# Performance work log

Hardware: AMD Instinct MI355X
Metric: run time of the kernel (lower is better)

## Reference

```python
import jax, jax.numpy as jnp
import numpy as np

TILE = 128  # pixel tile size, matches tile_pixels=128 default


def setup_inputs() -> dict:
    key = jax.random.key(0)
    ks = jax.random.split(key, 24)
    C, H, W, A, D, N, NC = 512, 32, 32, 256, 512, 1024, 30
    p = lambda k, s: (jax.random.normal(k, s, dtype=jnp.float32) * 0.02)
    return {
        "enc_out_nchw": jax.random.normal(ks[0], (1, C, H, W), dtype=jnp.float32),
        "tag_H": jax.random.normal(ks[1], (N, D), dtype=jnp.float32),
        # CellAttention linears ([in,out] layout)
        "W_enc": p(ks[2], (C, A)), "b_enc": p(ks[3], (A,)),
        "W_tag": p(ks[4], (D, A)), "b_tag": p(ks[5], (A,)),
        "W_lang": p(ks[6], (D, A)), "b_lang": p(ks[7], (A,)),
        "w_full": p(ks[8], (A,)), "b_full": p(ks[9], ()),
        # init hidden / gate
        "W_init": p(ks[10], (C, D)), "b_init": p(ks[11], (D,)),
        "W_fbeta": p(ks[12], (D, C)), "b_fbeta": p(ks[13], (C,)),
        # heads
        "W_cls": p(ks[14], (C, NC + 1)), "b_cls": p(ks[15], (NC + 1,)),
        "W_m1": p(ks[16], (C, 256)), "b_m1": p(ks[17], (256,)),
        "W_m2": p(ks[18], (256, 256)), "b_m2": p(ks[19], (256,)),
        "W_m3": p(ks[20], (256, 4)), "b_m3": p(ks[21], (4,)),
    }


def reference(enc_out_nchw, tag_H, W_enc, b_enc, W_tag, b_tag, W_lang, b_lang,
              w_full, b_full, W_init, b_init, W_fbeta, b_fbeta,
              W_cls, b_cls, W_m1, b_m1, W_m2, b_m2, W_m3, b_m3):
    C = enc_out_nchw.shape[1]
    enc_flat = enc_out_nchw[0].reshape(C, -1).T          # [P, C]
    P = enc_flat.shape[0]
    N = tag_H.shape[0]

    S_p = enc_flat @ W_enc + b_enc                       # [P, A]
    R_n = tag_H @ W_tag + b_tag                          # [N, A]
    mean_enc = enc_flat.mean(axis=0)                     # [C]
    h0 = mean_enc @ W_init + b_init                      # [D] (same row expanded to N in torch)
    L = h0 @ W_lang + b_lang                             # [A] (identical for all cells)
    RL = R_n + L                                         # [N, A]

    # tiled additive-attention scores; never materialize [N,P,A]
    T = P // TILE
    Sp_tiles = S_p.reshape(T, TILE, -1)                  # [T, TILE, A]

    def tile_score(_, sp_tile):
        z = jax.nn.relu(RL[:, None, :] + sp_tile[None, :, :]) @ w_full + b_full  # [N, TILE]
        return None, z

    _, Z = jax.lax.scan(tile_score, None, Sp_tiles)      # [T, N, TILE]
    Z = jnp.transpose(Z, (1, 0, 2)).reshape(N, P)        # [N, P]

    alpha = jax.nn.softmax(Z, axis=1)                    # streaming softmax == stable softmax
    awe = alpha @ enc_flat                               # [N, C]

    gate = jax.nn.sigmoid(h0 @ W_fbeta + b_fbeta)        # [C]
    h = gate * awe * h0                                  # [N, C]; dropout is identity at inference

    logits_cls = h @ W_cls + b_cls                       # [N, num_classes+1]
    x = jax.nn.relu(h @ W_m1 + b_m1)
    x = jax.nn.relu(x @ W_m2 + b_m2)
    boxes = jax.nn.sigmoid(x @ W_m3 + b_m3)              # [N, 4]
    return logits_cls, boxes
```

## Files before the change

kernel.cpp:

```cpp
#include <hip/hip_runtime.h>
#include <math.h>


__device__ __forceinline__ float4 ld4(const float* p) {
  return *reinterpret_cast<const float4*>(p);
}
__device__ __forceinline__ void st4(float* p, float4 v) {
  *reinterpret_cast<float4*>(p) = v;
}

__global__ void mean_kernel(const float* __restrict__ enc, float* __restrict__ mean) {
  const int c = blockIdx.x, t = threadIdx.x;
  float4 v = reinterpret_cast<const float4*>(enc + (size_t)c * 1024)[t];
  float s = v.x + v.y + v.z + v.w;
  #pragma unroll
  for (int off = 32; off; off >>= 1) s += __shfl_xor(s, off);
  __shared__ float red[4];
  if ((t & 63) == 0) red[t >> 6] = s;
  __syncthreads();
  if (t == 0) mean[c] = (red[0] + red[1] + red[2] + red[3]) * (1.0f / 1024.0f);
}

__global__ __launch_bounds__(256) void h0_k(
    const float* __restrict__ mean, const float* __restrict__ W_init,
    const float* __restrict__ b_init, float* __restrict__ h0) {
  __shared__ float ms[512];
  __shared__ float red[8][33];
  const int t = threadIdx.x;
  ms[t] = mean[t]; ms[t + 256] = mean[t + 256];
  __syncthreads();
  const int d0 = blockIdx.x * 32, dl = t & 31, cg = t >> 5;
  float acc = 0.f;
  #pragma unroll 8
  for (int c = cg * 64; c < cg * 64 + 64; ++c)
    acc += ms[c] * W_init[c * 512 + d0 + dl];
  red[cg][dl] = acc;
  __syncthreads();
  if (t < 32) {
    const float s = red[0][t] + red[1][t] + red[2][t] + red[3][t]
                  + red[4][t] + red[5][t] + red[6][t] + red[7][t];
    h0[d0 + t] = s + b_init[d0 + t];
  }
}

__global__ __launch_bounds__(256) void ghL_k(
    const float* __restrict__ h0, const float* __restrict__ W_fbeta,
    const float* __restrict__ b_fbeta, const float* __restrict__ W_lang,
    const float* __restrict__ b_lang, float* __restrict__ gh,
    float* __restrict__ Lv) {
  __shared__ float hs[512];
  __shared__ float red[8][33];
  const int t = threadIdx.x;
  hs[t] = h0[t]; hs[t + 256] = h0[t + 256];
  __syncthreads();
  const int b = blockIdx.x, ol = t & 31, cg = t >> 5;
  if (b < 16) {
    const int c0 = b * 32;
    float acc = 0.f;
    #pragma unroll 8
    for (int d = cg * 64; d < cg * 64 + 64; ++d)
      acc += hs[d] * W_fbeta[d * 512 + c0 + ol];
    red[cg][ol] = acc;
    __syncthreads();
    if (t < 32) {
      const int c = c0 + t;
      const float s = red[0][t] + red[1][t] + red[2][t] + red[3][t]
                    + red[4][t] + red[5][t] + red[6][t] + red[7][t] + b_fbeta[c];
      gh[c] = hs[c] / (1.f + __expf(-s));
    }
  } else {
    const int a0 = (b - 16) * 32;
    float acc = 0.f;
    #pragma unroll 8
    for (int d = cg * 64; d < cg * 64 + 64; ++d)
      acc += hs[d] * W_lang[d * 256 + a0 + ol];
    red[cg][ol] = acc;
    __syncthreads();
    if (t < 32) {
      const float s = red[0][t] + red[1][t] + red[2][t] + red[3][t]
                    + red[4][t] + red[5][t] + red[6][t] + red[7][t];
      Lv[a0 + t] = s + b_lang[a0 + t];
    }
  }
}

template <int AMODE, int BMODE, bool BIAS1, bool NEXACT>
__device__ __forceinline__ void gemm_body2(
    const float* __restrict__ A0, const float* __restrict__ A1,
    const float* __restrict__ A2, const float* __restrict__ A3,
    const float* __restrict__ avec, const float* __restrict__ B,
    const float* __restrict__ bias1, float* __restrict__ C,
    int M, int N, int K, int m0, int n0, int k0, int nsteps,
    float* As, float* Bs) {
  constexpr int LDA = 36, LDB = 68, NA = 8, NB = 16;
  const int tid = threadIdx.x;
  const int tx = tid & 15, ty = tid >> 4;
  float acc[2][4] = {{0.f, 0.f, 0.f, 0.f}, {0.f, 0.f, 0.f, 0.f}};
  float pa[NA], pb[NB];

  auto loadA = [&](int kk0) {
    #pragma unroll
    for (int i = 0; i < NA; ++i) {
      const int idx = tid + i * 256;
      if (AMODE == 1) {
        const int k = idx >> 5, mm = idx & 31;
        pa[i] = A0[(size_t)(kk0 + k) * M + m0 + mm];
      } else {
        const int k = idx & 63, mm = idx >> 6;
        const size_t off = (size_t)(m0 + mm) * K + kk0 + k;
        if (AMODE == 0) {
          pa[i] = A0[off];
        } else {
          float s = A0[off] + A1[off] + A2[off] + A3[off];
          if (AMODE == 2) pa[i] = avec[kk0 + k] * s;
          else            pa[i] = fmaxf(s + avec[kk0 + k], 0.f);
        }
      }
    }
  };
  auto loadB = [&](int kk0) {
    #pragma unroll
    for (int i = 0; i < NB; ++i) {
      const int idx = tid + i * 256;
      if (BMODE == 0) {
        const int k = idx >> 6, nn = idx & 63;
        pb[i] = (NEXACT || (n0 + nn < N)) ? B[(size_t)(kk0 + k) * N + n0 + nn] : 0.f;
      } else {
        const int k = idx & 63, nn = idx >> 6;
        pb[i] = B[(size_t)(n0 + nn) * K + kk0 + k];
      }
    }
  };
  auto storeAB = [&]() {
    #pragma unroll
    for (int i = 0; i < NA; ++i) {
      const int idx = tid + i * 256;
      if (AMODE == 1) { const int k = idx >> 5, mm = idx & 31; As[k * LDA + mm] = pa[i]; }
      else            { const int k = idx & 63, mm = idx >> 6; As[k * LDA + mm] = pa[i]; }
    }
    #pragma unroll
    for (int i = 0; i < NB; ++i) {
      const int idx = tid + i * 256;
      if (BMODE == 0) { const int k = idx >> 6, nn = idx & 63; Bs[k * LDB + nn] = pb[i]; }
      else            { const int k = idx & 63, nn = idx >> 6; Bs[k * LDB + nn] = pb[i]; }
    }
  };

  loadA(k0); loadB(k0);
  for (int ts = 0; ts < nsteps; ++ts) {
    storeAB();
    __syncthreads();
    if (ts + 1 < nsteps) { loadA(k0 + (ts + 1) * 64); loadB(k0 + (ts + 1) * 64); }
    #pragma unroll
    for (int k = 0; k < 64; ++k) {
      const float2 av = *reinterpret_cast<const float2*>(As + k * LDA + ty * 2);
      const float4 bv = *reinterpret_cast<const float4*>(Bs + k * LDB + tx * 4);
      acc[0][0] += av.x * bv.x; acc[0][1] += av.x * bv.y;
      acc[0][2] += av.x * bv.z; acc[0][3] += av.x * bv.w;
      acc[1][0] += av.y * bv.x; acc[1][1] += av.y * bv.y;
      acc[1][2] += av.y * bv.z; acc[1][3] += av.y * bv.w;
    }
    __syncthreads();
  }

  #pragma unroll
  for (int i = 0; i < 2; ++i) {
    const int mm = m0 + ty * 2 + i;
    #pragma unroll
    for (int j = 0; j < 4; ++j) {
      const int nn = n0 + tx * 4 + j;
      if (NEXACT || nn < N) {
        float v = acc[i][j];
        if (BIAS1) v += bias1[nn];
        C[(size_t)mm * N + nn] = v;
      }
    }
  }
}

template <int AMODE, int BMODE>
__device__ __forceinline__ void gemm_body4(
    const float* __restrict__ A0, const float* __restrict__ A1,
    const float* __restrict__ A2, const float* __restrict__ A3,
    const float* __restrict__ avec, const float* __restrict__ B,
    float* __restrict__ C,
    int M, int N, int K, int m0, int n0, int k0, int nsteps,
    float* As, float* Bs) {
  constexpr int LD = 68, NA = 16, NB = 16;
  const int tid = threadIdx.x;
  const int tx = tid & 15, ty = tid >> 4;
  float acc[4][4];
  #pragma unroll
  for (int i = 0; i < 4; ++i)
    #pragma unroll
    for (int j = 0; j < 4; ++j) acc[i][j] = 0.f;
  float pa[NA], pb[NB];

  auto loadA = [&](int kk0) {
    #pragma unroll
    for (int i = 0; i < NA; ++i) {
      const int idx = tid + i * 256;
      if (AMODE == 1) {
        const int k = idx >> 6, mm = idx & 63;
        pa[i] = A0[(size_t)(kk0 + k) * M + m0 + mm];
      } else {
        const int k = idx & 63, mm = idx >> 6;
        const size_t off = (size_t)(m0 + mm) * K + kk0 + k;
        if (AMODE == 0) {
          pa[i] = A0[off];
        } else {
          float s = A0[off] + A1[off] + A2[off] + A3[off];
          if (AMODE == 2) pa[i] = avec[kk0 + k] * s;
          else            pa[i] = fmaxf(s + avec[kk0 + k], 0.f);
        }
      }
    }
  };
  auto loadB = [&](int kk0) {
    #pragma unroll
    for (int i = 0; i < NB; ++i) {
      const int idx = tid + i * 256;
      if (BMODE == 0) {
        const int k = idx >> 6, nn = idx & 63;
        pb[i] = B[(size_t)(kk0 + k) * N + n0 + nn];
      } else {
        const int k = idx & 63, nn = idx >> 6;
        pb[i] = B[(size_t)(n0 + nn) * K + kk0 + k];
      }
    }
  };
  auto storeAB = [&]() {
    #pragma unroll
    for (int i = 0; i < NA; ++i) {
      const int idx = tid + i * 256;
      if (AMODE == 1) { const int k = idx >> 6, mm = idx & 63; As[k * LD + mm] = pa[i]; }
      else            { const int k = idx & 63, mm = idx >> 6; As[k * LD + mm] = pa[i]; }
    }
    #pragma unroll
    for (int i = 0; i < NB; ++i) {
      const int idx = tid + i * 256;
      if (BMODE == 0) { const int k = idx >> 6, nn = idx & 63; Bs[k * LD + nn] = pb[i]; }
      else            { const int k = idx & 63, nn = idx >> 6; Bs[k * LD + nn] = pb[i]; }
    }
  };

  loadA(k0); loadB(k0);
  for (int ts = 0; ts < nsteps; ++ts) {
    storeAB();
    __syncthreads();
    if (ts + 1 < nsteps) { loadA(k0 + (ts + 1) * 64); loadB(k0 + (ts + 1) * 64); }
    #pragma unroll
    for (int k = 0; k < 64; ++k) {
      const float4 av = *reinterpret_cast<const float4*>(As + k * LD + ty * 4);
      const float4 bv = *reinterpret_cast<const float4*>(Bs + k * LD + tx * 4);
      const float a4[4] = {av.x, av.y, av.z, av.w};
      const float b4[4] = {bv.x, bv.y, bv.z, bv.w};
      #pragma unroll
      for (int i = 0; i < 4; ++i)
        #pragma unroll
        for (int j = 0; j < 4; ++j) acc[i][j] += a4[i] * b4[j];
    }
    __syncthreads();
  }

  #pragma unroll
  for (int i = 0; i < 4; ++i) {
    const int mm = m0 + ty * 4 + i;
    float4 v; v.x = acc[i][0]; v.y = acc[i][1]; v.z = acc[i][2]; v.w = acc[i][3];
    st4(C + (size_t)mm * N + n0 + tx * 4, v);
  }
}

#define GEMM_LDS __shared__ float As[64 * 68]; __shared__ float Bs[64 * 68]

__global__ __launch_bounds__(256) void sprl2(
    const float* __restrict__ enc, const float* __restrict__ W_enc,
    const float* __restrict__ tagH, const float* __restrict__ W_tag,
    float* __restrict__ PS, float* __restrict__ PR) {
  GEMM_LDS;
  const int b = blockIdx.x;
  if (b < 256) {
    const int tile = b & 63, c = b >> 6;
    const int mi = tile & 3, ni = tile >> 2;
    gemm_body4<1, 0>(W_enc, nullptr, nullptr, nullptr, nullptr, enc,
        PS + c * 262144, 256, 1024, 512, mi * 64, ni * 64, c * 128, 2, As, Bs);
  } else {
    const int r = b - 256, tile = r & 63, c = r >> 6;
    const int mi = tile >> 2, ni = tile & 3;
    gemm_body4<0, 0>(tagH, nullptr, nullptr, nullptr, nullptr, W_tag,
        PR + c * 262144, 1024, 256, 512, mi * 64, ni * 64, c * 128, 2, As, Bs);
  }
}

__global__ void merge_k(const float* __restrict__ PS, const float* __restrict__ PR,
                        const float* __restrict__ b_enc, const float* __restrict__ b_tag,
                        const float* __restrict__ Lv, float* __restrict__ Sp,
                        float* __restrict__ RLm) {
  const int b = blockIdx.x, t = threadIdx.x;
  if (b < 256) {
    const size_t a = ((size_t)b * 256 + t) * 4;
    float4 s0 = ld4(PS + a), s1 = ld4(PS + 262144 + a);
    float4 s2 = ld4(PS + 524288 + a), s3 = ld4(PS + 786432 + a);
    float4 o;
    o.x = (s0.x + s1.x) + (s2.x + s3.x);
    o.y = (s0.y + s1.y) + (s2.y + s3.y);
    o.z = (s0.z + s1.z) + (s2.z + s3.z);
    o.w = (s0.w + s1.w) + (s2.w + s3.w);
    st4(Sp + a, o);
  } else {
    const size_t i = (size_t)(b - 256) * 256 + t;
    const size_t a = i * 4;
    const int a4 = (int)(i & 63) * 4;
    float4 s0 = ld4(PR + a), s1 = ld4(PR + 262144 + a);
    float4 s2 = ld4(PR + 524288 + a), s3 = ld4(PR + 786432 + a);
    const float4 be = ld4(b_enc + a4), bt = ld4(b_tag + a4), lv = ld4(Lv + a4);
    float4 o;
    o.x = (s0.x + s1.x) + (s2.x + s3.x) + be.x + bt.x + lv.x;
    o.y = (s0.y + s1.y) + (s2.y + s3.y) + be.y + bt.y + lv.y;
    o.z = (s0.z + s1.z) + (s2.z + s3.z) + be.z + bt.z + lv.z;
    o.w = (s0.w + s1.w) + (s2.w + s3.w) + be.w + bt.w + lv.w;
    st4(RLm + a, o);
  }
}

__global__ __launch_bounds__(256) void score4(
    const float* __restrict__ Sp, const float* __restrict__ RLm,
    const float* __restrict__ wfull, float* __restrict__ Zp) {
  __shared__ float spS[32][132];
  __shared__ float rlS[16][132];
  __shared__ float wS[128];
  const int b = blockIdx.x;
  const int h = b & 1, pt = (b >> 1) & 7, nt = b >> 4;
  const int n0 = nt * 16, p0 = pt * 128, a0 = h * 128;
  const int t = threadIdx.x, tx = t & 31, ty = t >> 5;

  {
    const int nn = t >> 4, ag = (t & 15) * 8;
    const float* src = RLm + (size_t)(n0 + nn) * 256 + a0 + ag;
    st4(&rlS[nn][ag], ld4(src));
    st4(&rlS[nn][ag + 4], ld4(src + 4));
  }
  if (t < 128) wS[t] = wfull[a0 + t];

  float4 pf[4];
  auto ldsp = [&](int ac) {
    #pragma unroll
    for (int i = 0; i < 4; ++i) {
      const int idx = t + i * 256;
      const int ar = idx >> 5, pc = (idx & 31) << 2;
      pf[i] = ld4(Sp + (size_t)(a0 + ac * 32 + ar) * 1024 + p0 + pc);
    }
  };

  float z[2][4] = {{0.f, 0.f, 0.f, 0.f}, {0.f, 0.f, 0.f, 0.f}};
  ldsp(0);
  for (int ac = 0; ac < 4; ++ac) {
    __syncthreads();
    #pragma unroll
    for (int i = 0; i < 4; ++i) {
      const int idx = t + i * 256;
      const int ar = idx >> 5, pc = (idx & 31) << 2;
      st4(&spS[ar][pc], pf[i]);
    }
    __syncthreads();
    if (ac < 3) ldsp(ac + 1);
    const int abase = ac * 32;
    #pragma unroll 8
    for (int al = 0; al < 32; ++al) {
      const float w = wS[abase + al];
      const float r0 = rlS[ty * 2][abase + al];
      const float r1 = rlS[ty * 2 + 1][abase + al];
      const float4 s = ld4(&spS[al][tx * 4]);
      z[0][0] += fmaxf(r0 + s.x, 0.f) * w;
      z[0][1] += fmaxf(r0 + s.y, 0.f) * w;
      z[0][2] += fmaxf(r0 + s.z, 0.f) * w;
      z[0][3] += fmaxf(r0 + s.w, 0.f) * w;
      z[1][0] += fmaxf(r1 + s.x, 0.f) * w;
      z[1][1] += fmaxf(r1 + s.y, 0.f) * w;
      z[1][2] += fmaxf(r1 + s.z, 0.f) * w;
      z[1][3] += fmaxf(r1 + s.w, 0.f) * w;
    }
  }

  #pragma unroll
  for (int i = 0; i < 2; ++i) {
    float4 o; o.x = z[i][0]; o.y = z[i][1]; o.z = z[i][2]; o.w = z[i][3];
    st4(Zp + (size_t)h * 1048576 + (size_t)(n0 + ty * 2 + i) * 1024 + p0 + tx * 4, o);
  }
}

__global__ __launch_bounds__(256) void softmax_k(const float* __restrict__ Zp,
                                                 float* __restrict__ alpha) {
  const int n = blockIdx.x, t = threadIdx.x;
  __shared__ float redm[4];
  __shared__ float reds[4];
  const size_t off = (size_t)n * 1024 + 4 * t;
  float4 z = ld4(Zp + off);
  const float4 a1 = ld4(Zp + 1048576 + off);
  z.x += a1.x; z.y += a1.y; z.z += a1.z; z.w += a1.w;
  float m = fmaxf(fmaxf(z.x, z.y), fmaxf(z.z, z.w));
  #pragma unroll
  for (int o = 32; o; o >>= 1) m = fmaxf(m, __shfl_xor(m, o));
  if ((t & 63) == 0) redm[t >> 6] = m;
  __syncthreads();
  m = fmaxf(fmaxf(redm[0], redm[1]), fmaxf(redm[2], redm[3]));
  z.x = __expf(z.x - m); z.y = __expf(z.y - m);
  z.z = __expf(z.z - m); z.w = __expf(z.w - m);
  float s = z.x + z.y + z.z + z.w;
  #pragma unroll
  for (int o = 32; o; o >>= 1) s += __shfl_xor(s, o);
  if ((t & 63) == 0) reds[t >> 6] = s;
  __syncthreads();
  s = reds[0] + reds[1] + reds[2] + reds[3];
  const float inv = 1.f / s;
  z.x *= inv; z.y *= inv; z.z *= inv; z.w *= inv;
  st4(alpha + off, z);
}

__global__ __launch_bounds__(256) void awe2(const float* __restrict__ alpha,
                                            const float* __restrict__ enc,
                                            float* __restrict__ PH) {
  GEMM_LDS;
  const int b = blockIdx.x, c = b >> 7, tile = b & 127;
  const int mi = tile >> 3, ni = tile & 7;
  gemm_body4<0, 1>(alpha, nullptr, nullptr, nullptr, nullptr, enc,
      PH + c * 524288, 1024, 512, 1024, mi * 64, ni * 64, c * 256, 4, As, Bs);
}

__global__ __launch_bounds__(256) void m1cls2(
    const float* __restrict__ PH, const float* __restrict__ gh,
    const float* __restrict__ W_m1, const float* __restrict__ W_cls,
    const float* __restrict__ b_cls, float* __restrict__ PX1,
    float* __restrict__ out) {
  GEMM_LDS;
  const int b = blockIdx.x;
  if (b < 32) {
    const int mi = b;
    gemm_body2<2, 0, true, false>(PH, PH + 524288, PH + 1048576, PH + 1572864, gh,
        W_cls, b_cls, out, 1024, 31, 512, mi * 32, 0, 0, 8, As, Bs);
  } else {
    const int r = b - 32, c = r >> 6, tile = r & 63;
    const int mi = tile >> 2, ni = tile & 3;
    gemm_body4<2, 0>(PH, PH + 524288, PH + 1048576, PH + 1572864, gh,
        W_m1, PX1 + c * 262144, 1024, 256, 512, mi * 64, ni * 64, c * 128, 2, As, Bs);
  }
}

__global__ __launch_bounds__(256) void m2k(
    const float* __restrict__ PX1, const float* __restrict__ b_m1,
    const float* __restrict__ W_m2, float* __restrict__ PX2) {
  GEMM_LDS;
  const int b = blockIdx.x;
  const int c = b >> 6, tile = b & 63, mi = tile >> 2, ni = tile & 3;
  gemm_body4<3, 0>(PX1, PX1 + 262144, PX1 + 524288, PX1 + 786432, b_m1,
      W_m2, PX2 + c * 262144, 1024, 256, 256, mi * 64, ni * 64, c * 64, 1, As, Bs);
}

__global__ __launch_bounds__(256) void m3k(
    const float* __restrict__ PX2, const float* __restrict__ b_m2,
    const float* __restrict__ W3, const float* __restrict__ b3,
    float* __restrict__ out2) {
  __shared__ float xr[8 * 260];
  __shared__ float w3s[1024];
  const int t = threadIdx.x, m0 = blockIdx.x * 8;
  #pragma unroll
  for (int ml = 0; ml < 8; ++ml) {
    const size_t off = (size_t)(m0 + ml) * 256 + t;
    const float s = PX2[off] + PX2[262144 + off] + PX2[524288 + off] + PX2[786432 + off]
                  + b_m2[t];
    xr[ml * 260 + t] = fmaxf(s, 0.f);
  }
  for (int i = t; i < 1024; i += 256) w3s[i] = W3[i];
  __syncthreads();
  if (t < 32) {
    const int ml = t >> 2, nn = t & 3;
    float acc = b3[nn];
    #pragma unroll 8
    for (int k = 0; k < 256; ++k) acc += xr[ml * 260 + k] * w3s[k * 4 + nn];
    out2[(size_t)(m0 + ml) * 4 + nn] = 1.f / (1.f + __expf(-acc));
  }
}

extern "C" void kernel_launch(void* const* d_in, const int* in_sizes, int n_in,
                              void* d_out, int out_size, void* d_ws, size_t ws_size,
                              hipStream_t stream) {
  const float* enc     = (const float*)d_in[0];
  const float* tagH    = (const float*)d_in[1];
  const float* W_enc   = (const float*)d_in[2];
  const float* b_enc   = (const float*)d_in[3];
  const float* W_tag   = (const float*)d_in[4];
  const float* b_tag   = (const float*)d_in[5];
  const float* W_lang  = (const float*)d_in[6];
  const float* b_lang  = (const float*)d_in[7];
  const float* w_full  = (const float*)d_in[8];
  const float* W_init  = (const float*)d_in[10];
  const float* b_init  = (const float*)d_in[11];
  const float* W_fbeta = (const float*)d_in[12];
  const float* b_fbeta = (const float*)d_in[13];
  const float* W_cls   = (const float*)d_in[14];
  const float* b_cls   = (const float*)d_in[15];
  const float* W_m1    = (const float*)d_in[16];
  const float* b_m1    = (const float*)d_in[17];
  const float* W_m2    = (const float*)d_in[18];
  const float* b_m2    = (const float*)d_in[19];
  const float* W_m3    = (const float*)d_in[20];
  const float* b_m3    = (const float*)d_in[21];
  float* out = (float*)d_out;

  float* ws    = (float*)d_ws;
  float* PS    = ws;
  float* PR    = ws + 1048576;
  float* alpha = ws;
  float* PX2   = ws;
  float* PX1   = ws + 1048576;
  float* Sp    = ws + 2097152;
  float* RLm   = ws + 2359296;
  float* Zp    = ws + 2621440;
  float* PH    = ws + 2621440;
  float* meanv = ws + 4718592;
  float* h0v   = ws + 4719104;
  float* Lv    = ws + 4719616;
  float* gh    = ws + 4719872;

  mean_kernel<<<512, 256, 0, stream>>>(enc, meanv);
  h0_k<<<16, 256, 0, stream>>>(meanv, W_init, b_init, h0v);
  ghL_k<<<24, 256, 0, stream>>>(h0v, W_fbeta, b_fbeta, W_lang, b_lang, gh, Lv);
  sprl2<<<512, 256, 0, stream>>>(enc, W_enc, tagH, W_tag, PS, PR);
  merge_k<<<512, 256, 0, stream>>>(PS, PR, b_enc, b_tag, Lv, Sp, RLm);
  score4<<<1024, 256, 0, stream>>>(Sp, RLm, w_full, Zp);
  softmax_k<<<1024, 256, 0, stream>>>(Zp, alpha);
  awe2<<<512, 256, 0, stream>>>(alpha, enc, PH);
  m1cls2<<<288, 256, 0, stream>>>(PH, gh, W_m1, W_cls, b_cls, PX1, out);
  m2k<<<256, 256, 0, stream>>>(PX1, b_m1, W_m2, PX2);
  m3k<<<128, 256, 0, stream>>>(PX2, b_m2, W_m3, b_m3, out + 31744);
}
```

Measured before the change: 224.4 us.

## Fuse mean into projection GEMM, shrink its tiles, split-K the classifier head

Result: faster. 209.1 us (-6.8%).

```diff
diff --git a/kernel.cpp b/kernel.cpp
--- a/kernel.cpp
+++ b/kernel.cpp
@@ -7,18 +7,6 @@
 }
 __device__ __forceinline__ void st4(float* p, float4 v) {
   *reinterpret_cast<float4*>(p) = v;
-}
-
-__global__ void mean_kernel(const float* __restrict__ enc, float* __restrict__ mean) {
-  const int c = blockIdx.x, t = threadIdx.x;
-  float4 v = reinterpret_cast<const float4*>(enc + (size_t)c * 1024)[t];
-  float s = v.x + v.y + v.z + v.w;
-  #pragma unroll
-  for (int off = 32; off; off >>= 1) s += __shfl_xor(s, off);
-  __shared__ float red[4];
-  if ((t & 63) == 0) red[t >> 6] = s;
-  __syncthreads();
-  if (t == 0) mean[c] = (red[0] + red[1] + red[2] + red[3]) * (1.0f / 1024.0f);
 }
 
 __global__ __launch_bounds__(256) void h0_k(
@@ -271,24 +259,32 @@
   }
 }
 
-#define GEMM_LDS __shared__ float As[64 * 68]; __shared__ float Bs[64 * 68]
-
-__global__ __launch_bounds__(256) void sprl2(
+__global__ __launch_bounds__(256) void sprlmean(
     const float* __restrict__ enc, const float* __restrict__ W_enc,
     const float* __restrict__ tagH, const float* __restrict__ W_tag,
-    float* __restrict__ PS, float* __restrict__ PR) {
-  GEMM_LDS;
+    float* __restrict__ PS, float* __restrict__ PR, float* __restrict__ mean) {
+  __shared__ float As[64 * 36];
+  __shared__ float Bs[64 * 68];
   const int b = blockIdx.x;
-  if (b < 256) {
-    const int tile = b & 63, c = b >> 6;
-    const int mi = tile & 3, ni = tile >> 2;
-    gemm_body4<1, 0>(W_enc, nullptr, nullptr, nullptr, nullptr, enc,
-        PS + c * 262144, 256, 1024, 512, mi * 64, ni * 64, c * 128, 2, As, Bs);
+  if (b < 512) {
+    const int tile = b & 127, c = b >> 7;
+    const int mi = tile & 7, ni = tile >> 3;
+    gemm_body2<1, 0, false, true>(W_enc, nullptr, nullptr, nullptr, nullptr, enc,
+        nullptr, PS + c * 262144, 256, 1024, 512, mi * 32, ni * 64, c * 128, 2, As, Bs);
+  } else if (b < 1024) {
+    const int r = b - 512, tile = r & 127, c = r >> 7;
+    const int mi = tile >> 2, ni = tile & 3;
+    gemm_body2<0, 0, false, true>(tagH, nullptr, nullptr, nullptr, nullptr, W_tag,
+        nullptr, PR + c * 262144, 1024, 256, 512, mi * 32, ni * 64, c * 128, 2, As, Bs);
   } else {
-    const int r = b - 256, tile = r & 63, c = r >> 6;
-    const int mi = tile >> 2, ni = tile & 3;
-    gemm_body4<0, 0>(tagH, nullptr, nullptr, nullptr, nullptr, W_tag,
-        PR + c * 262144, 1024, 256, 512, mi * 64, ni * 64, c * 128, 2, As, Bs);
+    const int c = b - 1024, t = threadIdx.x;
+    float4 v = reinterpret_cast<const float4*>(enc + (size_t)c * 1024)[t];
+    float s = v.x + v.y + v.z + v.w;
+    #pragma unroll
+    for (int off = 32; off; off >>= 1) s += __shfl_xor(s, off);
+    if ((t & 63) == 0) As[t >> 6] = s;
+    __syncthreads();
+    if (t == 0) mean[c] = (As[0] + As[1] + As[2] + As[3]) * (1.0f / 1024.0f);
   }
 }
 
@@ -420,7 +416,8 @@
 __global__ __launch_bounds__(256) void awe2(const float* __restrict__ alpha,
                                             const float* __restrict__ enc,
                                             float* __restrict__ PH) {
-  GEMM_LDS;
+  __shared__ float As[64 * 68];
+  __shared__ float Bs[64 * 68];
   const int b = blockIdx.x, c = b >> 7, tile = b & 127;
   const int mi = tile >> 3, ni = tile & 7;
   gemm_body4<0, 1>(alpha, nullptr, nullptr, nullptr, nullptr, enc,
@@ -430,16 +427,16 @@
 __global__ __launch_bounds__(256) void m1cls2(
     const float* __restrict__ PH, const float* __restrict__ gh,
     const float* __restrict__ W_m1, const float* __restrict__ W_cls,
-    const float* __restrict__ b_cls, float* __restrict__ PX1,
-    float* __restrict__ out) {
-  GEMM_LDS;
+    float* __restrict__ PX1, float* __restrict__ PC) {
+  __shared__ float As[64 * 68];
+  __shared__ float Bs[64 * 68];
   const int b = blockIdx.x;
-  if (b < 32) {
-    const int mi = b;
-    gemm_body2<2, 0, true, false>(PH, PH + 524288, PH + 1048576, PH + 1572864, gh,
-        W_cls, b_cls, out, 1024, 31, 512, mi * 32, 0, 0, 8, As, Bs);
+  if (b < 64) {
+    const int c = b >> 5, mi = b & 31;
+    gemm_body2<2, 0, false, false>(PH, PH + 524288, PH + 1048576, PH + 1572864, gh,
+        W_cls, nullptr, PC + c * 31744, 1024, 31, 512, mi * 32, 0, c * 256, 4, As, Bs);
   } else {
-    const int r = b - 32, c = r >> 6, tile = r & 63;
+    const int r = b - 64, c = r >> 6, tile = r & 63;
     const int mi = tile >> 2, ni = tile & 3;
     gemm_body4<2, 0>(PH, PH + 524288, PH + 1048576, PH + 1572864, gh,
         W_m1, PX1 + c * 262144, 1024, 256, 512, mi * 64, ni * 64, c * 128, 2, As, Bs);
@@ -449,7 +446,8 @@
 __global__ __launch_bounds__(256) void m2k(
     const float* __restrict__ PX1, const float* __restrict__ b_m1,
     const float* __restrict__ W_m2, float* __restrict__ PX2) {
-  GEMM_LDS;
+  __shared__ float As[64 * 68];
+  __shared__ float Bs[64 * 68];
   const int b = blockIdx.x;
   const int c = b >> 6, tile = b & 63, mi = tile >> 2, ni = tile & 3;
   gemm_body4<3, 0>(PX1, PX1 + 262144, PX1 + 524288, PX1 + 786432, b_m1,
@@ -459,25 +457,39 @@
 __global__ __launch_bounds__(256) void m3k(
     const float* __restrict__ PX2, const float* __restrict__ b_m2,
     const float* __restrict__ W3, const float* __restrict__ b3,
-    float* __restrict__ out2) {
-  __shared__ float xr[8 * 260];
-  __shared__ float w3s[1024];
-  const int t = threadIdx.x, m0 = blockIdx.x * 8;
-  #pragma unroll
-  for (int ml = 0; ml < 8; ++ml) {
-    const size_t off = (size_t)(m0 + ml) * 256 + t;
-    const float s = PX2[off] + PX2[262144 + off] + PX2[524288 + off] + PX2[786432 + off]
-                  + b_m2[t];
-    xr[ml * 260 + t] = fmaxf(s, 0.f);
-  }
-  for (int i = t; i < 1024; i += 256) w3s[i] = W3[i];
-  __syncthreads();
-  if (t < 32) {
-    const int ml = t >> 2, nn = t & 3;
-    float acc = b3[nn];
-    #pragma unroll 8
-    for (int k = 0; k < 256; ++k) acc += xr[ml * 260 + k] * w3s[k * 4 + nn];
-    out2[(size_t)(m0 + ml) * 4 + nn] = 1.f / (1.f + __expf(-acc));
+    const float* __restrict__ PC, const float* __restrict__ b_cls,
+    float* __restrict__ out_cls, float* __restrict__ out2) {
+  const int t = threadIdx.x, b = blockIdx.x;
+  if (b < 128) {
+    __shared__ float xr[8 * 260];
+    __shared__ float w3s[1024];
+    const int m0 = b * 8;
+    #pragma unroll
+    for (int ml = 0; ml < 8; ++ml) {
+      const size_t off = (size_t)(m0 + ml) * 256 + t;
+      const float s = PX2[off] + PX2[262144 + off] + PX2[524288 + off]
+                    + PX2[786432 + off] + b_m2[t];
+      xr[ml * 260 + t] = fmaxf(s, 0.f);
+    }
+    for (int i = t; i < 1024; i += 256) w3s[i] = W3[i];
+    __syncthreads();
+    if (t < 32) {
+      const int ml = t >> 2, nn = t & 3;
+      float acc = b3[nn];
+      #pragma unroll 8
+      for (int k = 0; k < 256; ++k) acc += xr[ml * 260 + k] * w3s[k * 4 + nn];
+      out2[(size_t)(m0 + ml) * 4 + nn] = 1.f / (1.f + __expf(-acc));
+    }
+  } else {
+    const int r8 = t >> 5, col = t & 31;
+    if (col < 31) {
+      const int mbase = (b - 128) * 32;
+      #pragma unroll
+      for (int i = 0; i < 4; ++i) {
+        const int m = mbase + r8 + i * 8;
+        out_cls[m * 31 + col] = PC[m * 31 + col] + PC[31744 + m * 31 + col] + b_cls[col];
+      }
+    }
   }
 }
 
@@ -521,16 +533,16 @@
   float* h0v   = ws + 4719104;
   float* Lv    = ws + 4719616;
   float* gh    = ws + 4719872;
-
-  mean_kernel<<<512, 256, 0, stream>>>(enc, meanv);
+  float* PC    = ws + 4720384;
+
+  sprlmean<<<1536, 256, 0, stream>>>(enc, W_enc, tagH, W_tag, PS, PR, meanv);
   h0_k<<<16, 256, 0, stream>>>(meanv, W_init, b_init, h0v);
   ghL_k<<<24, 256, 0, stream>>>(h0v, W_fbeta, b_fbeta, W_lang, b_lang, gh, Lv);
-  sprl2<<<512, 256, 0, stream>>>(enc, W_enc, tagH, W_tag, PS, PR);
   merge_k<<<512, 256, 0, stream>>>(PS, PR, b_enc, b_tag, Lv, Sp, RLm);
   score4<<<1024, 256, 0, stream>>>(Sp, RLm, w_full, Zp);
   softmax_k<<<1024, 256, 0, stream>>>(Zp, alpha);
   awe2<<<512, 256, 0, stream>>>(alpha, enc, PH);
-  m1cls2<<<288, 256, 0, stream>>>(PH, gh, W_m1, W_cls, b_cls, PX1, out);
+  m1cls2<<<320, 256, 0, stream>>>(PH, gh, W_m1, W_cls, PX1, PC);
   m2k<<<256, 256, 0, stream>>>(PX1, b_m1, W_m2, PX2);
-  m3k<<<128, 256, 0, stream>>>(PX2, b_m2, W_m3, b_m3, out + 31744);
-}
+  m3k<<<160, 256, 0, stream>>>(PX2, b_m2, W_m3, b_m3, PC, b_cls, out, out + 31744);
+}
```
